# Performance work log

Measured on AMD Instinct MI355X. Metric: run time of the kernel, lower is better.

Reference implementation:

```python
import jax, jax.numpy as jnp
import numpy as np

N, E, IN, H, T = 100000, 1600000, 10, 64, 10


def setup_inputs() -> dict:
    key = jax.random.key(0)
    ks = jax.random.split(key, 24)
    w = lambda k, shape, s=0.05: jax.random.normal(k, shape, jnp.float32) * s
    return {
        "x": w(ks[0], (N, IN), 1.0),
        "edge_attr": w(ks[1], (E, T), 1.0),
        "gcn1_w": w(ks[2], (IN, H)), "gcn1_b": jnp.zeros((H,), jnp.float32),
        "e_w1": w(ks[3], (3 * T, H)), "e_b1": jnp.zeros((H,), jnp.float32),
        "e_w2": w(ks[4], (H, H)), "e_b2": jnp.zeros((H,), jnp.float32),
        "gcn2_w": w(ks[5], (2 * H, H)), "gcn2_b": jnp.zeros((H,), jnp.float32),
        "gcn3_w": w(ks[6], (H, IN)), "gcn3_b": jnp.zeros((IN,), jnp.float32),
        "l1_w": w(ks[7], (2 * IN, IN)), "l1_b": jnp.zeros((IN,), jnp.float32),
        "l2_w": w(ks[8], (IN, 128)), "l2_b": jnp.zeros((128,), jnp.float32),
        "l3_w": w(ks[9], (128, 32)), "l3_b": jnp.zeros((32,), jnp.float32),
        "l4_w": w(ks[10], (32, 2)), "l4_b": jnp.zeros((2,), jnp.float32),
        "edge_index": jax.random.randint(ks[11], (2, E), 0, N),
    }


def reference(x, edge_attr, gcn1_w, gcn1_b, e_w1, e_b1, e_w2, e_b2,
              gcn2_w, gcn2_b, gcn3_w, gcn3_b, l1_w, l1_b, l2_w, l2_b,
              l3_w, l3_b, l4_w, l4_b, edge_index):
    src, dst = edge_index[0], edge_index[1]  # j -> i (message flows src->dst)
    # GCN symmetric norm with self loops: deg counted on target, +1 self loop
    deg = 1.0 + jax.ops.segment_sum(jnp.ones((E,), jnp.float32), dst, num_segments=N)
    dis = deg ** -0.5  # [N]
    edge_norm = (dis[src] * dis[dst])[:, None]  # [E,1]

    def gcn(h, w, b):
        hw = h @ w  # [N,out]
        agg = jax.ops.segment_sum(hw[src] * edge_norm, dst, num_segments=N)
        agg = agg + hw * (dis * dis)[:, None]  # self-loop term, norm = 1/deg
        return agg + b

    out1 = jax.nn.relu(gcn(x, gcn1_w, gcn1_b))
    # EdgeConv: gather x_i (dst), x_j (src), concat edge_attr, MLP, scatter-max
    m = jnp.concatenate([x[dst], x[src], edge_attr], axis=1)  # [E, 3T]
    m = jax.nn.relu(m @ e_w1 + e_b1) @ e_w2 + e_b2  # [E, H]
    agg = jax.ops.segment_max(m, dst, num_segments=N)
    agg = jnp.where(jnp.isfinite(agg), agg, 0.0)  # isolated nodes -> 0
    oute = jax.nn.relu(agg)

    out2 = jax.nn.relu(gcn(jnp.concatenate([out1, oute], axis=1), gcn2_w, gcn2_b))
    out3 = jax.nn.relu(gcn(out2, gcn3_w, gcn3_b))
    h = jnp.concatenate([x, out3], axis=1)  # [N, 2*IN]
    h = jax.nn.softplus(h @ l1_w + l1_b)
    h = jax.nn.softplus(h @ l2_w + l2_b)
    h = jax.nn.softplus(h @ l3_w + l3_b)
    h = h @ l4_w + l4_b  # [N, 2]
    return (h[:, 0], h[:, 1])
```

## Files before the change

### kernel.cpp

```cpp
#include <hip/hip_runtime.h>
#include <hip/hip_bf16.h>

typedef unsigned int u32;
typedef unsigned short u16;
typedef _Float16 f16;
typedef _Float16 f16x8 __attribute__((ext_vector_type(8)));
typedef float f32x4 __attribute__((ext_vector_type(4)));
typedef u32 u32x4 __attribute__((ext_vector_type(4)));

#define DEV static __device__ __forceinline__

#define O_G1   0
#define O_G1b  640
#define O_W1   704
#define O_B1   2624
#define O_W2   2688
#define O_B2   6784
#define O_G2   6848
#define O_G2b  15040
#define O_G3   15104
#define O_G3b  15744
#define O_L1   15754
#define O_L1b  15954
#define O_L2t  15964
#define O_L2b  17244
#define O_L3   17372
#define O_L3b  21468
#define O_L4t  21500
#define O_L4b  21564
#define O_WF1  21568
#define O_WF2  22592
#define WTOT   24640

#define ECNB   32

DEV float bfu(u16 h){ return __uint_as_float(((u32)h) << 16); }
DEV float bflo(u32 u){ return __uint_as_float(u << 16); }
DEV float bfhi(u32 u){ return __uint_as_float(u & 0xffff0000u); }
DEV u16 f2bf(float x){
  __hip_bfloat16 b = __float2bfloat16(x);
  return *(u16*)&b;
}
DEV float rdf(const void* p, int idx, int isf32){
  return isf32 ? ((const float*)p)[idx] : bfu(((const u16*)p)[idx]);
}
DEV void load10_bf(const u32* __restrict__ p, float* f){
  u32 a0=p[0],a1=p[1],a2=p[2],a3=p[3],a4=p[4];
  f[0]=bflo(a0); f[1]=bfhi(a0);
  f[2]=bflo(a1); f[3]=bfhi(a1);
  f[4]=bflo(a2); f[5]=bfhi(a2);
  f[6]=bflo(a3); f[7]=bfhi(a3);
  f[8]=bflo(a4); f[9]=bfhi(a4);
}
DEV void load10_any(const void* base, size_t row, int isf32, float* f){
  if (isf32){
    const float* p = (const float*)base + row*10;
    #pragma unroll
    for (int k=0;k<10;k++) f[k] = p[k];
  } else {
    load10_bf((const u32*)base + row*5, f);
  }
}
DEV float softplusf(float x){ return fmaxf(x,0.f) + __logf(1.f + __expf(-fabsf(x))); }

DEV int permk(int k){
  if (k < 8)  return k;
  if (k < 16) return 10 + (k-8);
  if (k < 24) return 20 + (k-16);
  if (k == 24) return 8;
  if (k == 25) return 9;
  if (k == 26) return 18;
  if (k == 27) return 19;
  if (k == 28) return 28;
  if (k == 29) return 29;
  return -1;
}
DEV u32 packh2(float a, float b){
  union { f16 h[2]; u32 u; } t;
  t.h[0] = (f16)a; t.h[1] = (f16)b;
  return t.u;
}

__global__ __launch_bounds__(256) void k_detect(
    const u32* p0, const u32* p1, const u32* p2, const u32* p3,
    const u32* p4, const u32* p5, const u32* p6, const u32* p7,
    const u32* p8, const u32* p9, const u32* p10,const u32* p11,
    const u32* p12,const u32* p13,const u32* p14,const u32* p15,
    const u32* p16,const u32* p17,const u32* p18,const u32* p19,
    int* __restrict__ flags, int N_, int E_)
{
  int a = blockIdx.x;
  const u32* p;
  int elems;
  switch (a){
    case 0:  p=p0;  elems=N_*10; break;
    case 1:  p=p1;  elems=E_*10; break;
    case 2:  p=p2;  elems=640;  break;
    case 3:  p=p3;  elems=64;   break;
    case 4:  p=p4;  elems=1920; break;
    case 5:  p=p5;  elems=64;   break;
    case 6:  p=p6;  elems=4096; break;
    case 7:  p=p7;  elems=64;   break;
    case 8:  p=p8;  elems=8192; break;
    case 9:  p=p9;  elems=64;   break;
    case 10: p=p10; elems=640;  break;
    case 11: p=p11; elems=10;   break;
    case 12: p=p12; elems=200;  break;
    case 13: p=p13; elems=10;   break;
    case 14: p=p14; elems=1280; break;
    case 15: p=p15; elems=128;  break;
    case 16: p=p16; elems=4096; break;
    case 17: p=p17; elems=32;   break;
    case 18: p=p18; elems=64;   break;
    default: p=p19; elems=2;    break;
  }
  int nw = elems/2; if (nw > 512) nw = 512; if (nw < 1) nw = 1;
  int localA = 0, localZ = 0;
  for (int i=threadIdx.x; i<nw; i+=256){
    u32 w = p[i];
    u32 ex = (w >> 7) & 0xffu;
    if (ex >= 0x90u) localA++;
    if ((w & 0xffffu) == 0u) localZ++;
  }
  int packed = (localA << 16) | localZ;
  __shared__ int red[4];
  #pragma unroll
  for (int off=32; off; off>>=1) packed += __shfl_down(packed, off);
  if ((threadIdx.x & 63) == 0) red[threadIdx.x>>6] = packed;
  __syncthreads();
  if (threadIdx.x == 0){
    int s = red[0]+red[1]+red[2]+red[3];
    int sA = s >> 16, sZ = s & 0xffff;
    flags[a] = (sA * 16 >= nw || sZ * 4 >= nw * 3) ? 1 : 0;
  }
}

__global__ __launch_bounds__(256) void k_prep(
    const void* g1w, const void* g1b, const void* ew1, const void* eb1,
    const void* ew2, const void* eb2, const void* g2w, const void* g2b,
    const void* g3w, const void* g3b, const void* l1w, const void* l1b,
    const void* l2w, const void* l2b, const void* l3w, const void* l3b,
    const void* l4w, const void* l4b,
    const int* __restrict__ flags, float* __restrict__ W)
{
  int t = threadIdx.x;
  int f2=flags[2],f3=flags[3],f4=flags[4],f5=flags[5],f6=flags[6],f7=flags[7];
  int f8=flags[8],f9=flags[9],f10=flags[10],f11=flags[11],f12=flags[12],f13=flags[13];
  int f14=flags[14],f15=flags[15],f16=flags[16],f17=flags[17],f18=flags[18],f19=flags[19];
  for (int i=t;i<640;i+=256)  W[O_G1+i]  = rdf(g1w,i,f2);
  for (int i=t;i<64;i+=256)   W[O_G1b+i] = rdf(g1b,i,f3);
  for (int i=t;i<1920;i+=256) W[O_W1+i]  = rdf(ew1,i,f4);
  for (int i=t;i<64;i+=256)   W[O_B1+i]  = rdf(eb1,i,f5);
  for (int i=t;i<4096;i+=256) W[O_W2+i]  = rdf(ew2,i,f6);
  for (int i=t;i<64;i+=256)   W[O_B2+i]  = rdf(eb2,i,f7);
  for (int i=t;i<8192;i+=256) W[O_G2+i]  = rdf(g2w,i,f8);
  for (int i=t;i<64;i+=256)   W[O_G2b+i] = rdf(g2b,i,f9);
  for (int i=t;i<640;i+=256)  W[O_G3+i]  = rdf(g3w,i,f10);
  for (int i=t;i<10;i+=256)   W[O_G3b+i] = rdf(g3b,i,f11);
  for (int i=t;i<200;i+=256)  W[O_L1+i]  = rdf(l1w,i,f12);
  for (int i=t;i<10;i+=256)   W[O_L1b+i] = rdf(l1b,i,f13);
  for (int i=t;i<1280;i+=256){ int o=i/10,k=i-o*10; W[O_L2t+i]=rdf(l2w,k*128+o,f14); }
  for (int i=t;i<128;i+=256)  W[O_L2b+i] = rdf(l2b,i,f15);
  for (int i=t;i<4096;i+=256) W[O_L3+i]  = rdf(l3w,i,f16);
  for (int i=t;i<32;i+=256)   W[O_L3b+i] = rdf(l3b,i,f17);
  for (int i=t;i<64;i+=256){ int c=i>>5,j=i&31; W[O_L4t+i]=rdf(l4w,j*2+c,f18); }
  for (int i=t;i<2;i+=256)    W[O_L4b+i] = rdf(l4b,i,f19);
  u32* Wu = (u32*)W;
  for (int i=t;i<1024;i+=256){
    int l=i&63, q=(i>>6)&3, c=i>>8;
    int k0=(l>>4)*8+2*q, col=c*16+(l&15);
    int r0=permk(k0), r1=permk(k0+1);
    float v0 = (r0<0)?0.f:rdf(ew1,r0*64+col,f4);
    float v1 = (r1<0)?0.f:rdf(ew1,r1*64+col,f4);
    Wu[O_WF1+i] = packh2(v0,v1);
  }
  for (int i=t;i<2048;i+=256){
    int l=i&63, q=(i>>6)&3, h2=(i>>8)&1, c=i>>9;
    int k0=32*h2+(l>>4)*8+2*q, col=c*16+(l&15);
    Wu[O_WF2+i] = packh2(rdf(ew2,k0*64+col,f6), rdf(ew2,(k0+1)*64+col,f6));
  }
}

__global__ __launch_bounds__(256) void k_init(int* __restrict__ cnt, int N_)
{
  int i = blockIdx.x*256 + threadIdx.x;
  if (i < N_) cnt[i] = 0;
}

__global__ __launch_bounds__(256) void k_count(
    const int* __restrict__ ei, int* __restrict__ cnt,
    int* __restrict__ rank, int E_)
{
  int e = blockIdx.x*256 + threadIdx.x;
  if (e >= E_) return;
  rank[e] = atomicAdd(&cnt[ei[E_+e]], 1);
}

__global__ __launch_bounds__(1024) void k_bsum(const int* __restrict__ cnt, int* __restrict__ bsum, int N_)
{
  int i = blockIdx.x*1024 + threadIdx.x;
  int v = (i < N_) ? cnt[i] : 0;
  #pragma unroll
  for (int off=32; off; off>>=1) v += __shfl_down(v, off);
  __shared__ int ws_[16];
  if ((threadIdx.x & 63) == 0) ws_[threadIdx.x>>6] = v;
  __syncthreads();
  if (threadIdx.x == 0){
    int s = 0;
    #pragma unroll
    for (int j=0;j<16;j++) s += ws_[j];
    bsum[blockIdx.x] = s;
  }
}

__global__ __launch_bounds__(128) void k_scan_small(const int* __restrict__ bsum, int* __restrict__ boff, int NB)
{
  int t = threadIdx.x;
  int v = (t < NB) ? bsum[t] : 0;
  int lane = t & 63, w = t >> 6;
  int x = v;
  #pragma unroll
  for (int off=1; off<64; off<<=1){ int y=__shfl_up(x,off); if (lane>=off) x+=y; }
  __shared__ int t2[2];
  if (lane==63) t2[w]=x;
  __syncthreads();
  if (w==1) x += t2[0];
  boff[t] = x - v;
}

__global__ __launch_bounds__(1024) void k_scan_final(
    int* __restrict__ cnt, const int* __restrict__ boff,
    int* __restrict__ rp, float* __restrict__ dis, int N_, int E_)
{
  int i = blockIdx.x*1024 + threadIdx.x;
  int v = (i < N_) ? cnt[i] : 0;
  int lane = threadIdx.x & 63, w = threadIdx.x >> 6;
  int x = v;
  #pragma unroll
  for (int off=1; off<64; off<<=1){ int y=__shfl_up(x,off); if (lane>=off) x+=y; }
  __shared__ int wp[16];
  if (lane==63) wp[w]=x;
  __syncthreads();
  if (threadIdx.x==0){
    int run=0;
    #pragma unroll
    for (int j=0;j<16;j++){ int t=wp[j]; wp[j]=run; run+=t; }
  }
  __syncthreads();
  int incl = x + wp[w] + boff[blockIdx.x];
  if (i < N_){
    rp[i]  = incl - v;
    dis[i] = rsqrtf(1.f + (float)v);
  }
  if (i == 0) rp[N_] = E_;
}

__global__ __launch_bounds__(256) void k_fillpos(
    const int* __restrict__ ei, const int* __restrict__ rank,
    const int* __restrict__ rp, int* __restrict__ inv, int E_)
{
  int e = blockIdx.x*256 + threadIdx.x;
  if (e >= E_) return;
  int d = ei[E_+e];
  inv[rp[d] + rank[e]] = e;
}

__global__ __launch_bounds__(256) void k_fillcsr(
    const int* __restrict__ ei, const int* __restrict__ inv,
    int4* __restrict__ csr, int E_)
{
  int p = blockIdx.x*256 + threadIdx.x;
  if (p >= E_) return;
  int e = inv[p];
  csr[p] = make_int4(ei[e], e, ei[E_+e], 0);
}

#define EC_EMIT \
  if (run >= 0){ int bb = run*64 + x; \
    atomicMax(&nodemax[bb],    __float_as_int(e0)); \
    atomicMax(&nodemax[bb+16], __float_as_int(e1)); \
    atomicMax(&nodemax[bb+32], __float_as_int(e2)); \
    atomicMax(&nodemax[bb+48], __float_as_int(e3)); }
#define EC_STEP(DD, RR) { \
  float t0=fmaxf(mcv[0][RR],0.f), t1=fmaxf(mcv[1][RR],0.f), \
        t2=fmaxf(mcv[2][RR],0.f), t3=fmaxf(mcv[3][RR],0.f); \
  if (DD == run){ e0=fmaxf(e0,t0); e1=fmaxf(e1,t1); e2=fmaxf(e2,t2); e3=fmaxf(e3,t3); } \
  else { EC_EMIT; run = DD; e0=t0; e1=t1; e2=t2; e3=t3; } }

__global__ __launch_bounds__(256) void k_edgeconv(
    const void* __restrict__ xv, const void* __restrict__ eav,
    const int* __restrict__ rp, const int4* __restrict__ csr,
    const float* __restrict__ W, const int* __restrict__ flags,
    float* __restrict__ oute, int N_, int E_)
{
  __shared__ int nodemax[ECNB*64];
  __shared__ u32 hbuf[4][16*36];
  int tid = threadIdx.x;
  int l = tid & 63, wv = tid >> 6;
  int x = l & 15, g = l >> 4;
  int n0 = blockIdx.x * ECNB;
  if (n0 >= N_) return;
  int nend = n0 + ECNB; if (nend > N_) nend = N_;
  #pragma unroll
  for (int i=0;i<ECNB/4;i++) nodemax[i*256 + tid] = 0;
  int fx = flags[0], fea = flags[1];
  const u32* Wu = (const u32*)W;
  union FU { u32 u[4]; f16x8 v; };
  union HU { f16 h[8]; u32 u[4]; f16x8 v; };
  FU w1u[4];
  #pragma unroll
  for (int c=0;c<4;c++){
    #pragma unroll
    for (int q=0;q<4;q++) w1u[c].u[q] = Wu[O_WF1 + (c*4+q)*64 + l];
  }
  FU w2u[4][2];
  #pragma unroll
  for (int c=0;c<4;c++){
    #pragma unroll
    for (int h=0;h<2;h++){
      #pragma unroll
      for (int q=0;q<4;q++) w2u[c][h].u[q] = Wu[O_WF2 + ((c*2+h)*4+q)*64 + l];
    }
  }
  float b1v[4], b2v[4];
  #pragma unroll
  for (int c=0;c<4;c++){ b1v[c] = (W+O_B1)[c*16 + x]; b2v[c] = (W+O_B2)[c*16 + x]; }
  int pbase = rp[n0], pend = rp[nend];
  int ntiles = (pend - pbase + 15) >> 4;
  u32* hb = hbuf[wv];
  __syncthreads();

  for (int t = wv; t < ntiles; t += 4){
    int p0 = pbase + t*16;
    int eA = p0 + x; if (eA > E_-1) eA = E_-1;
    int4 ce = csr[eA];
    HU af;
    u32 exv = 0;
    if (g < 3){
      long row; const void* base; int isf;
      if (g==0){ row = ce.z; base = xv;  isf = fx; }
      else if (g==1){ row = ce.x; base = xv;  isf = fx; }
      else { row = ce.y; base = eav; isf = fea; }
      if (isf){
        const float* p = (const float*)base + row*10;
        #pragma unroll
        for (int j=0;j<8;j++) af.h[j] = (f16)p[j];
        exv = packh2(p[8], p[9]);
      } else {
        const u32* p = (const u32*)base + row*5;
        u32 a0=p[0],a1=p[1],a2=p[2],a3=p[3],a4=p[4];
        af.h[0]=(f16)bflo(a0); af.h[1]=(f16)bfhi(a0);
        af.h[2]=(f16)bflo(a1); af.h[3]=(f16)bfhi(a1);
        af.h[4]=(f16)bflo(a2); af.h[5]=(f16)bfhi(a2);
        af.h[6]=(f16)bflo(a3); af.h[7]=(f16)bfhi(a3);
        exv = packh2(bflo(a4), bfhi(a4));
      }
    }
    u32 ge0 = (u32)__shfl((int)exv, x);
    u32 ge1 = (u32)__shfl((int)exv, x+16);
    u32 ge2 = (u32)__shfl((int)exv, x+32);
    if (g == 3){ af.u[0]=ge0; af.u[1]=ge1; af.u[2]=ge2; af.u[3]=0; }
    int pe = p0 + 4*g;
    int dz = ce.z;
    int d0 = __shfl(dz, 4*g+0); d0 = (pe   < pend) ? d0 - n0 : -1;
    int d1 = __shfl(dz, 4*g+1); d1 = (pe+1 < pend) ? d1 - n0 : -1;
    int d2 = __shfl(dz, 4*g+2); d2 = (pe+2 < pend) ? d2 - n0 : -1;
    int d3 = __shfl(dz, 4*g+3); d3 = (pe+3 < pend) ? d3 - n0 : -1;
    f32x4 z = {0.f,0.f,0.f,0.f};
    f32x4 hc[4];
    #pragma unroll
    for (int c=0;c<4;c++)
      hc[c] = __builtin_amdgcn_mfma_f32_16x16x32_f16(af.v, w1u[c].v, z, 0, 0, 0);
    #pragma unroll
    for (int r=0;r<4;r++){
      u32 pk0,pk1,pk2,pk3;
      {
        float hv = fmaxf(hc[0][r] + b1v[0], 0.f);
        union { f16 h; u16 u; } cv; cv.h=(f16)hv; u32 mine=cv.u;
        u32 other=(u32)__shfl_xor((int)mine,1,64);
        pk0 = (x&1) ? (other|(mine<<16)) : (mine|(other<<16));
      }{
        float hv = fmaxf(hc[1][r] + b1v[1], 0.f);
        union { f16 h; u16 u; } cv; cv.h=(f16)hv; u32 mine=cv.u;
        u32 other=(u32)__shfl_xor((int)mine,1,64);
        pk1 = (x&1) ? (other|(mine<<16)) : (mine|(other<<16));
      }{
        float hv = fmaxf(hc[2][r] + b1v[2], 0.f);
        union { f16 h; u16 u; } cv; cv.h=(f16)hv; u32 mine=cv.u;
        u32 other=(u32)__shfl_xor((int)mine,1,64);
        pk2 = (x&1) ? (other|(mine<<16)) : (mine|(other<<16));
      }{
        float hv = fmaxf(hc[3][r] + b1v[3], 0.f);
        union { f16 h; u16 u; } cv; cv.h=(f16)hv; u32 mine=cv.u;
        u32 other=(u32)__shfl_xor((int)mine,1,64);
        pk3 = (x&1) ? (other|(mine<<16)) : (mine|(other<<16));
      }
      int edge = 4*g + r;
      int par = (x&1) ? 16 : 0;
      hb[edge*36 + par + (x>>1)]     = (x&1) ? pk2 : pk0;
      hb[edge*36 + 8 + par + (x>>1)] = (x&1) ? pk3 : pk1;
    }
    asm volatile("s_waitcnt lgkmcnt(0)" ::: "memory");
    HU a2f[2];
    #pragma unroll
    for (int h=0;h<2;h++){
      const u32x4* p = (const u32x4*)&hb[x*36 + g*4 + 16*h];
      u32x4 tv = *p;
      a2f[h].u[0]=tv[0]; a2f[h].u[1]=tv[1]; a2f[h].u[2]=tv[2]; a2f[h].u[3]=tv[3];
    }
    f32x4 mcv[4];
    #pragma unroll
    for (int c=0;c<4;c++){
      f32x4 bi = {b2v[c],b2v[c],b2v[c],b2v[c]};
      f32x4 acc = __builtin_amdgcn_mfma_f32_16x16x32_f16(a2f[0].v, w2u[c][0].v, bi, 0, 0, 0);
      mcv[c]    = __builtin_amdgcn_mfma_f32_16x16x32_f16(a2f[1].v, w2u[c][1].v, acc, 0, 0, 0);
    }
    int run = -2; float e0=0.f,e1=0.f,e2=0.f,e3=0.f;
    EC_STEP(d0,0) EC_STEP(d1,1) EC_STEP(d2,2) EC_STEP(d3,3)
    EC_EMIT;
  }
  __syncthreads();
  int tot = (nend - n0) * 64;
  for (int i = tid; i < tot; i += 256)
    oute[(size_t)n0*64 + i] = __int_as_float(nodemax[i]);
}

__global__ __launch_bounds__(256) void k_aggxhw2(
    const void* __restrict__ xv, const int* __restrict__ rp,
    const int4* __restrict__ csr, const float* __restrict__ dis,
    const int* __restrict__ flags, const float* __restrict__ oute,
    const float* __restrict__ W, u16* __restrict__ hw2o, int N_)
{
  int i = blockIdx.x*256 + threadIdx.x;
  if (i >= N_) return;
  int fx = flags[0];
  float di = dis[i], d2 = di*di;
  float sv[10], ac2[10], tA[10], tB[10], tC[10], tD[10];
  load10_any(xv, (size_t)i, fx, tA);
  #pragma unroll
  for (int f=0;f<10;f++){ sv[f] = tA[f]*d2; ac2[f] = 0.f; }
  int b = rp[i], en = rp[i+1];
  int p = b;
  for (; p+3 < en; p += 4){
    int s0 = csr[p].x, s1 = csr[p+1].x, s2 = csr[p+2].x, s3 = csr[p+3].x;
    float m0 = dis[s0]*di, m1 = dis[s1]*di, m2 = dis[s2]*di, m3 = dis[s3]*di;
    load10_any(xv, (size_t)s0, fx, tA);
    load10_any(xv, (size_t)s1, fx, tB);
    load10_any(xv, (size_t)s2, fx, tC);
    load10_any(xv, (size_t)s3, fx, tD);
    #pragma unroll
    for (int f=0;f<10;f++){
      sv[f]  = fmaf(tA[f], m0, sv[f]);
      ac2[f] = fmaf(tB[f], m1, ac2[f]);
      sv[f]  = fmaf(tC[f], m2, sv[f]);
      ac2[f] = fmaf(tD[f], m3, ac2[f]);
    }
  }
  for (; p < en; p++){
    int s0 = csr[p].x; float m0 = dis[s0]*di;
    load10_any(xv, (size_t)s0, fx, tA);
    #pragma unroll
    for (int f=0;f<10;f++) sv[f] = fmaf(tA[f], m0, sv[f]);
  }
  #pragma unroll
  for (int f=0;f<10;f++) sv[f] += ac2[f];
  const float* __restrict__ G1  = W + O_G1;
  const float* __restrict__ G1b = W + O_G1b;
  const float* __restrict__ G2  = W + O_G2;
  float hw[64];
  #pragma unroll
  for (int f=0;f<64;f++) hw[f] = 0.f;
  #pragma unroll 1
  for (int k=0;k<64;k++){
    float o1 = G1b[k];
    #pragma unroll
    for (int j=0;j<10;j++) o1 = fmaf(sv[j], G1[j*64+k], o1);
    o1 = fmaxf(o1, 0.f);
    const float* __restrict__ wt = G2 + k*64;
    #pragma unroll
    for (int f=0;f<64;f++) hw[f] = fmaf(o1, wt[f], hw[f]);
  }
  const float* orow = oute + (size_t)i*64;
  #pragma unroll 1
  for (int k=0;k<64;k++){
    float ov = orow[k];
    const float* __restrict__ wb = G2 + (64+k)*64;
    #pragma unroll
    for (int f=0;f<64;f++) hw[f] = fmaf(ov, wb[f], hw[f]);
  }
  u16* out = hw2o + (size_t)i*64;
  #pragma unroll
  for (int f=0;f<64;f++) out[f] = f2bf(hw[f]);
}

__global__ __launch_bounds__(256) void k_agg64(
    const u16* __restrict__ hw2, const int* __restrict__ rp,
    const int4* __restrict__ csr, const float* __restrict__ dis,
    const float* __restrict__ W, float* __restrict__ out2, int N_)
{
  int i = (blockIdx.x*256 + threadIdx.x) >> 6;
  int lane = threadIdx.x & 63;
  if (i >= N_) return;
  int e4 = lane >> 4, c4 = lane & 15;
  float di = dis[i];
  int b = rp[i], en = rp[i+1];
  const uint2* __restrict__ h2 = (const uint2*)hw2;
  float a0=0.f,a1=0.f,a2=0.f,a3=0.f;
  float b0=0.f,b1=0.f,b2=0.f,b3=0.f;
  int p = b + e4;
  int sA = (p   < en) ? csr[p].x   : 0;
  int sB = (p+4 < en) ? csr[p+4].x : 0;
  for (; p + 4 < en; p += 8){
    int sAn = (p+8  < en) ? csr[p+8].x  : 0;
    int sBn = (p+12 < en) ? csr[p+12].x : 0;
    float nmA = dis[sA]*di, nmB = dis[sB]*di;
    uint2 wA = h2[(size_t)sA*16 + c4];
    uint2 wB = h2[(size_t)sB*16 + c4];
    a0 = fmaf(bflo(wA.x), nmA, a0); a1 = fmaf(bfhi(wA.x), nmA, a1);
    a2 = fmaf(bflo(wA.y), nmA, a2); a3 = fmaf(bfhi(wA.y), nmA, a3);
    b0 = fmaf(bflo(wB.x), nmB, b0); b1 = fmaf(bfhi(wB.x), nmB, b1);
    b2 = fmaf(bflo(wB.y), nmB, b2); b3 = fmaf(bfhi(wB.y), nmB, b3);
    sA = sAn; sB = sBn;
  }
  if (p < en){
    float nmA = dis[sA]*di;
    uint2 wA = h2[(size_t)sA*16 + c4];
    a0 = fmaf(bflo(wA.x), nmA, a0); a1 = fmaf(bfhi(wA.x), nmA, a1);
    a2 = fmaf(bflo(wA.y), nmA, a2); a3 = fmaf(bfhi(wA.y), nmA, a3);
  }
  a0 += b0; a1 += b1; a2 += b2; a3 += b3;
  a0 += __shfl_xor(a0,16); a1 += __shfl_xor(a1,16);
  a2 += __shfl_xor(a2,16); a3 += __shfl_xor(a3,16);
  a0 += __shfl_xor(a0,32); a1 += __shfl_xor(a1,32);
  a2 += __shfl_xor(a2,32); a3 += __shfl_xor(a3,32);
  if (e4 == 0){
    uint2 ws2 = h2[(size_t)i*16 + c4];
    float d2 = di*di;
    const float* G2b = W + O_G2b;
    float4 o;
    o.x = fmaxf(fmaf(bflo(ws2.x), d2, a0) + G2b[4*c4],   0.f);
    o.y = fmaxf(fmaf(bfhi(ws2.x), d2, a1) + G2b[4*c4+1], 0.f);
    o.z = fmaxf(fmaf(bflo(ws2.y), d2, a2) + G2b[4*c4+2], 0.f);
    o.w = fmaxf(fmaf(bfhi(ws2.y), d2, a3) + G2b[4*c4+3], 0.f);
    *(float4*)(out2 + (size_t)i*64 + 4*c4) = o;
  }
}

__global__ __launch_bounds__(256) void k_hw3(
    const float* __restrict__ out2, const float* __restrict__ W,
    float* __restrict__ hw3, int N_)
{
  int i = blockIdx.x*256 + threadIdx.x;
  if (i >= N_) return;
  const float* row = out2 + (size_t)i*64;
  const float* __restrict__ G3 = W + O_G3;
  float a[10];
  #pragma unroll
  for (int f=0;f<10;f++) a[f] = 0.f;
  #pragma unroll 1
  for (int k=0;k<64;k++){
    float v = row[k];
    const float* __restrict__ w = G3 + k*10;
    #pragma unroll
    for (int f=0;f<10;f++) a[f] = fmaf(v, w[f], a[f]);
  }
  float* o = hw3 + (size_t)i*10;
  #pragma unroll
  for (int f=0;f<10;f++) o[f] = a[f];
}

__global__ __launch_bounds__(256) void k_final(
    const void* __restrict__ xv, const float* __restrict__ hw3,
    const int* __restrict__ rp, const int4* __restrict__ csr,
    const float* __restrict__ dis, const int* __restrict__ flags,
    const float* __restrict__ W, float* __restrict__ out, int N_)
{
  int i = blockIdx.x*256 + threadIdx.x;
  if (i >= N_) return;
  int fx = flags[0];
  float di = dis[i];
  float a[10], a2v[10];
  const float* hrow = hw3 + (size_t)i*10;
  #pragma unroll
  for (int f=0;f<10;f++){ a[f] = hrow[f]*di*di; a2v[f] = 0.f; }
  int b = rp[i], en = rp[i+1];
  int p = b;
  for (; p+3 < en; p += 4){
    int s0 = csr[p].x, s1 = csr[p+1].x, s2 = csr[p+2].x, s3 = csr[p+3].x;
    float m0 = dis[s0]*di, m1 = dis[s1]*di, m2 = dis[s2]*di, m3 = dis[s3]*di;
    const float* r0p = hw3 + (size_t)s0*10;
    const float* r1p = hw3 + (size_t)s1*10;
    const float* r2p = hw3 + (size_t)s2*10;
    const float* r3p = hw3 + (size_t)s3*10;
    #pragma unroll
    for (int f=0;f<10;f++){
      a[f]   = fmaf(r0p[f], m0, a[f]);
      a2v[f] = fmaf(r1p[f], m1, a2v[f]);
      a[f]   = fmaf(r2p[f], m2, a[f]);
      a2v[f] = fmaf(r3p[f], m3, a2v[f]);
    }
  }
  for (; p < en; p++){
    int s0 = csr[p].x; float m0 = dis[s0]*di;
    const float* r0p = hw3 + (size_t)s0*10;
    #pragma unroll
    for (int f=0;f<10;f++) a[f] = fmaf(r0p[f], m0, a[f]);
  }
  #pragma unroll
  for (int f=0;f<10;f++) a[f] += a2v[f];
  const float* G3b = W + O_G3b;
  float h20[20];
  load10_any(xv, (size_t)i, fx, h20);
  #pragma unroll
  for (int f=0;f<10;f++) h20[10+f] = fmaxf(a[f] + G3b[f], 0.f);
  const float* __restrict__ L1  = W + O_L1;
  const float* __restrict__ L1b = W + O_L1b;
  float h1[10];
  #pragma unroll
  for (int f=0;f<10;f++) h1[f] = L1b[f];
  #pragma unroll
  for (int k=0;k<20;k++){
    float v = h20[k];
    const float* __restrict__ w = L1 + k*10;
    #pragma unroll
    for (int f=0;f<10;f++) h1[f] = fmaf(v, w[f], h1[f]);
  }
  #pragma unroll
  for (int f=0;f<10;f++) h1[f] = softplusf(h1[f]);
  const float* __restrict__ L2t = W + O_L2t;
  const float* __restrict__ L2b = W + O_L2b;
  const float* __restrict__ L3  = W + O_L3;
  const float* __restrict__ L3b = W + O_L3b;
  float h3a[32], h3b[32];
  #pragma unroll
  for (int j=0;j<32;j++){ h3a[j] = L3b[j]; h3b[j] = 0.f; }
  #pragma unroll 1
  for (int o=0;o<64;o++){
    float sA = L2b[o], sB = L2b[o+64];
    const float* __restrict__ wtA = L2t + o*10;
    const float* __restrict__ wtB = L2t + (o+64)*10;
    #pragma unroll
    for (int k=0;k<10;k++){
      sA = fmaf(h1[k], wtA[k], sA);
      sB = fmaf(h1[k], wtB[k], sB);
    }
    sA = softplusf(sA);
    sB = softplusf(sB);
    const float* __restrict__ w3A = L3 + o*32;
    const float* __restrict__ w3B = L3 + (o+64)*32;
    #pragma unroll
    for (int j=0;j<32;j++){
      h3a[j] = fmaf(sA, w3A[j], h3a[j]);
      h3b[j] = fmaf(sB, w3B[j], h3b[j]);
    }
  }
  const float* L4t = W + O_L4t;
  const float* L4b = W + O_L4b;
  float r0 = L4b[0], r1 = L4b[1];
  #pragma unroll
  for (int j=0;j<32;j++){
    float h3 = softplusf(h3a[j] + h3b[j]);
    r0 = fmaf(h3, L4t[j],    r0);
    r1 = fmaf(h3, L4t[32+j], r1);
  }
  out[i]      = r0;
  out[N_ + i] = r1;
}

extern "C" void kernel_launch(void* const* d_in, const int* in_sizes, int n_in,
                              void* d_out, int out_size, void* d_ws, size_t ws_size,
                              hipStream_t stream)
{
  const void* xv  = d_in[0];
  const void* eav = d_in[1];
  const int*  ei  = (const int*)d_in[20];
  int N_ = in_sizes[0] / 10;
  int E_ = in_sizes[1] / 10;

  float* W = (float*)d_ws;
  size_t off = WTOT;
  int*   cnt   = (int*)(W + off);   off += (size_t)N_;
  int*   rp    = (int*)(W + off);   off += (size_t)N_ + 1;
  float* dis   = (float*)(W + off); off += (size_t)N_;
  int*   bsum  = (int*)(W + off);   off += 256;
  int*   boff  = (int*)(W + off);   off += 256;
  int*   flags = (int*)(W + off);   off += 32;
  off = (off + 3) & ~(size_t)3;
  int4*  csr   = (int4*)(W + off);  off += (size_t)E_ * 4;
  float* oute  = (float*)(W + off); off += (size_t)N_ * 64;
  float* out2  = oute;
  u16*   hw2   = (u16*)(W + off);   off += (size_t)N_ * 32;
  float* hw3   = (float*)(W + off); off += (size_t)N_ * 10;

  int* rank;
  if ((size_t)E_ <= (size_t)N_ * 64) rank = (int*)oute;
  else { rank = (int*)(W + off); off += (size_t)E_; }
  int* inv;
  if ((size_t)E_ <= (size_t)N_ * 32) inv = (int*)hw2;
  else { inv = (int*)(W + off); off += (size_t)E_; }

  if (ws_size < off * sizeof(float)) return;

  int gN = (N_ + 255)/256, gE = (E_ + 255)/256;
  int NB = (N_ + 1023)/1024;

  k_detect<<<20,256,0,stream>>>(
      (const u32*)d_in[0],(const u32*)d_in[1],
      (const u32*)d_in[2],(const u32*)d_in[3],(const u32*)d_in[4],(const u32*)d_in[5],
      (const u32*)d_in[6],(const u32*)d_in[7],(const u32*)d_in[8],(const u32*)d_in[9],
      (const u32*)d_in[10],(const u32*)d_in[11],(const u32*)d_in[12],(const u32*)d_in[13],
      (const u32*)d_in[14],(const u32*)d_in[15],(const u32*)d_in[16],(const u32*)d_in[17],
      (const u32*)d_in[18],(const u32*)d_in[19],
      flags, N_, E_);
  k_prep<<<1,256,0,stream>>>(
      d_in[2],d_in[3],d_in[4],d_in[5],d_in[6],d_in[7],d_in[8],d_in[9],
      d_in[10],d_in[11],d_in[12],d_in[13],d_in[14],d_in[15],d_in[16],d_in[17],
      d_in[18],d_in[19], flags, W);
  k_init<<<gN,256,0,stream>>>(cnt, N_);
  k_count<<<gE,256,0,stream>>>(ei, cnt, rank, E_);
  k_bsum<<<NB,1024,0,stream>>>(cnt, bsum, N_);
  k_scan_small<<<1,128,0,stream>>>(bsum, boff, NB);
  k_scan_final<<<NB,1024,0,stream>>>(cnt, boff, rp, dis, N_, E_);
  k_fillpos<<<gE,256,0,stream>>>(ei, rank, rp, inv, E_);
  k_fillcsr<<<gE,256,0,stream>>>(ei, inv, csr, E_);
  k_edgeconv<<<(N_+ECNB-1)/ECNB,256,0,stream>>>(xv, eav, rp, csr, W, flags, oute, N_, E_);
  k_aggxhw2<<<gN,256,0,stream>>>(xv, rp, csr, dis, flags, oute, W, hw2, N_);
  k_agg64<<<(N_+3)/4,256,0,stream>>>(hw2, rp, csr, dis, W, out2, N_);
  k_hw3<<<gN,256,0,stream>>>(out2, W, hw3, N_);
  k_final<<<gN,256,0,stream>>>(xv, hw3, rp, csr, dis, flags, W,
                               (float*)d_out, N_);
}
```

Baseline: 644.6 us.

## Shrink CSR to int2 and pre-permute edge attributes into fp16 CSR order

The CSR entry drops the edge id and padding, shrinking it from int4 to int2, which reduces the bytes read by every aggregation kernel. The fill kernel now also gathers edge_attr into CSR order, already converted to packed fp16. EdgeConv can then read those attributes contiguously instead of through a random gather by edge id. The cost is an extra E*5-word buffer written during CSR construction, and the random gather moves into k_fillcsr.

Result: slower. 665.4 us (+3.2%).

```diff
diff --git a/kernel.cpp b/kernel.cpp
--- a/kernel.cpp
+++ b/kernel.cpp
@@ -267,12 +267,24 @@
 
 __global__ __launch_bounds__(256) void k_fillcsr(
     const int* __restrict__ ei, const int* __restrict__ inv,
-    int4* __restrict__ csr, int E_)
+    const int* __restrict__ flags, const void* __restrict__ eav,
+    int2* __restrict__ csr, u32* __restrict__ ea2, int E_)
 {
   int p = blockIdx.x*256 + threadIdx.x;
   if (p >= E_) return;
   int e = inv[p];
-  csr[p] = make_int4(ei[e], e, ei[E_+e], 0);
+  csr[p] = make_int2(ei[e], ei[E_+e]);
+  int fea = flags[1];
+  u32* o = ea2 + (size_t)p*5;
+  if (fea){
+    const float* q = (const float*)eav + (size_t)e*10;
+    #pragma unroll
+    for (int j=0;j<5;j++) o[j] = packh2(q[2*j], q[2*j+1]);
+  } else {
+    const u32* q = (const u32*)eav + (size_t)e*5;
+    #pragma unroll
+    for (int j=0;j<5;j++){ u32 w = q[j]; o[j] = packh2(bflo(w), bfhi(w)); }
+  }
 }
 
 #define EC_EMIT \
@@ -288,8 +300,8 @@
   else { EC_EMIT; run = DD; e0=t0; e1=t1; e2=t2; e3=t3; } }
 
 __global__ __launch_bounds__(256) void k_edgeconv(
-    const void* __restrict__ xv, const void* __restrict__ eav,
-    const int* __restrict__ rp, const int4* __restrict__ csr,
+    const void* __restrict__ xv, const u32* __restrict__ ea2,
+    const int* __restrict__ rp, const int2* __restrict__ csr,
     const float* __restrict__ W, const int* __restrict__ flags,
     float* __restrict__ oute, int N_, int E_)
 {
@@ -303,7 +315,7 @@
   int nend = n0 + ECNB; if (nend > N_) nend = N_;
   #pragma unroll
   for (int i=0;i<ECNB/4;i++) nodemax[i*256 + tid] = 0;
-  int fx = flags[0], fea = flags[1];
+  int fx = flags[0];
   const u32* Wu = (const u32*)W;
   union FU { u32 u[4]; f16x8 v; };
   union HU { f16 h[8]; u32 u[4]; f16x8 v; };
@@ -333,21 +345,22 @@
   for (int t = wv; t < ntiles; t += 4){
     int p0 = pbase + t*16;
     int eA = p0 + x; if (eA > E_-1) eA = E_-1;
-    int4 ce = csr[eA];
+    int2 ce = csr[eA];
     HU af;
     u32 exv = 0;
-    if (g < 3){
-      long row; const void* base; int isf;
-      if (g==0){ row = ce.z; base = xv;  isf = fx; }
-      else if (g==1){ row = ce.x; base = xv;  isf = fx; }
-      else { row = ce.y; base = eav; isf = fea; }
-      if (isf){
-        const float* p = (const float*)base + row*10;
+    if (g == 2){
+      const u32* q = ea2 + (size_t)eA*5;
+      af.u[0]=q[0]; af.u[1]=q[1]; af.u[2]=q[2]; af.u[3]=q[3];
+      exv = q[4];
+    } else if (g < 2){
+      long row = (g==0) ? (long)ce.y : (long)ce.x;
+      if (fx){
+        const float* p = (const float*)xv + row*10;
         #pragma unroll
         for (int j=0;j<8;j++) af.h[j] = (f16)p[j];
         exv = packh2(p[8], p[9]);
       } else {
-        const u32* p = (const u32*)base + row*5;
+        const u32* p = (const u32*)xv + row*5;
         u32 a0=p[0],a1=p[1],a2=p[2],a3=p[3],a4=p[4];
         af.h[0]=(f16)bflo(a0); af.h[1]=(f16)bfhi(a0);
         af.h[2]=(f16)bflo(a1); af.h[3]=(f16)bfhi(a1);
@@ -361,7 +374,7 @@
     u32 ge2 = (u32)__shfl((int)exv, x+32);
     if (g == 3){ af.u[0]=ge0; af.u[1]=ge1; af.u[2]=ge2; af.u[3]=0; }
     int pe = p0 + 4*g;
-    int dz = ce.z;
+    int dz = ce.y;
     int d0 = __shfl(dz, 4*g+0); d0 = (pe   < pend) ? d0 - n0 : -1;
     int d1 = __shfl(dz, 4*g+1); d1 = (pe+1 < pend) ? d1 - n0 : -1;
     int d2 = __shfl(dz, 4*g+2); d2 = (pe+2 < pend) ? d2 - n0 : -1;
@@ -427,7 +440,7 @@
 
 __global__ __launch_bounds__(256) void k_aggxhw2(
     const void* __restrict__ xv, const int* __restrict__ rp,
-    const int4* __restrict__ csr, const float* __restrict__ dis,
+    const int2* __restrict__ csr, const float* __restrict__ dis,
     const int* __restrict__ flags, const float* __restrict__ oute,
     const float* __restrict__ W, u16* __restrict__ hw2o, int N_)
 {
@@ -495,7 +508,7 @@
 
 __global__ __launch_bounds__(256) void k_agg64(
     const u16* __restrict__ hw2, const int* __restrict__ rp,
-    const int4* __restrict__ csr, const float* __restrict__ dis,
+    const int2* __restrict__ csr, const float* __restrict__ dis,
     const float* __restrict__ W, float* __restrict__ out2, int N_)
 {
   int i = (blockIdx.x*256 + threadIdx.x) >> 6;
@@ -571,7 +584,7 @@
 
 __global__ __launch_bounds__(256) void k_final(
     const void* __restrict__ xv, const float* __restrict__ hw3,
-    const int* __restrict__ rp, const int4* __restrict__ csr,
+    const int* __restrict__ rp, const int2* __restrict__ csr,
     const float* __restrict__ dis, const int* __restrict__ flags,
     const float* __restrict__ W, float* __restrict__ out, int N_)
 {
@@ -686,7 +699,8 @@
   int*   boff  = (int*)(W + off);   off += 256;
   int*   flags = (int*)(W + off);   off += 32;
   off = (off + 3) & ~(size_t)3;
-  int4*  csr   = (int4*)(W + off);  off += (size_t)E_ * 4;
+  int2*  csr   = (int2*)(W + off);  off += (size_t)E_ * 2;
+  u32*   ea2   = (u32*)(W + off);   off += (size_t)E_ * 5;
   float* oute  = (float*)(W + off); off += (size_t)N_ * 64;
   float* out2  = oute;
   u16*   hw2   = (u16*)(W + off);   off += (size_t)N_ * 32;
@@ -722,8 +736,8 @@
   k_scan_small<<<1,128,0,stream>>>(bsum, boff, NB);
   k_scan_final<<<NB,1024,0,stream>>>(cnt, boff, rp, dis, N_, E_);
   k_fillpos<<<gE,256,0,stream>>>(ei, rank, rp, inv, E_);
-  k_fillcsr<<<gE,256,0,stream>>>(ei, inv, csr, E_);
-  k_edgeconv<<<(N_+ECNB-1)/ECNB,256,0,stream>>>(xv, eav, rp, csr, W, flags, oute, N_, E_);
+  k_fillcsr<<<gE,256,0,stream>>>(ei, inv, flags, eav, csr, ea2, E_);
+  k_edgeconv<<<(N_+ECNB-1)/ECNB,256,0,stream>>>(xv, ea2, rp, csr, W, flags, oute, N_, E_);
   k_aggxhw2<<<gN,256,0,stream>>>(xv, rp, csr, dis, flags, oute, W, hw2, N_);
   k_agg64<<<(N_+3)/4,256,0,stream>>>(hw2, rp, csr, dis, W, out2, N_);
   k_hw3<<<gN,256,0,stream>>>(out2, W, hw3, N_);
```
